# Kernel optimization log

Measured on AMD Instinct MI355X. Metric: run time of the kernel, lower is better.

Reference implementation:

```python
import jax, jax.numpy as jnp
import numpy as np

B, D, Nh, L = 8, 128, 8, 1024
Dk = D // Nh  # 16
Dv = D // Nh  # 16

def _xavier(key, shape):
    # nn.init.xavier_normal_ on a 3D tensor treats dim0 as fan irrelevant:
    # fan_in = shape[-1]*1, fan_out = shape[-2]*1 for >=2D; receptive field = prod(shape[2:])? For 3D torch uses
    # fan_in = shape[1]*shape[2]? We just need same distribution family; use std from last two dims.
    fan_in, fan_out = shape[-1], shape[-2]
    std = float(np.sqrt(2.0 / (fan_in + fan_out)))
    return jax.random.normal(key, shape, dtype=jnp.float32) * std

def setup_inputs() -> dict:
    key = jax.random.key(0)
    kx, kq, kk, kv, ko = jax.random.split(key, 5)
    x = jax.random.normal(kx, (B, D, L), dtype=jnp.float32)
    Wq = _xavier(kq, (Nh, B, Dk, D))
    Wk = _xavier(kk, (Nh, B, Dk, D))
    Wv = _xavier(kv, (Nh, B, Dv, D))
    Wo = _xavier(ko, (B, Dv * Nh, D))
    return {"x": x, "Wq": Wq, "Wk": Wk, "Wv": Wv, "Wo": Wo}

def reference(x, Wq, Wk, Wv, Wo):
    scale = 1.0 / np.sqrt(Dk)
    # Project all heads at once: [Nh,B,Dk,D] x [B,D,L] -> [B,Nh,Dk,L]
    Q = jnp.einsum('hbkd,bdl->bhkl', Wq, x)
    K = jnp.einsum('hbkd,bdl->bhkl', Wk, x)
    V = jnp.einsum('hbvd,bdl->bhvl', Wv, x)
    # scores[b,h,i,j] = sum_k Q[b,h,k,i] * K[b,h,k,j]
    scores = jnp.einsum('bhki,bhkj->bhij', Q, K) * scale
    # original softmaxes over dim=1 of [B,L,L] -> the i (Q-length) axis
    attn = jax.nn.softmax(scores, axis=2)
    # head[b,h,v,j] = sum_i V[b,h,v,i] * attn[b,h,i,j]
    head = jnp.einsum('bhvi,bhij->bhvj', V, attn)
    # concat heads along channel dim (order matches torch.cat over head list)
    head = head.reshape(B, Nh * Dv, L)
    # Wo [B, Nh*Dv, D] bmm head [B, D(=Nh*Dv), L] -> [B, Nh*Dv, L]
    out = jnp.einsum('bod,bdl->bol', Wo, head)
    return out
```

## Files before the change

kernel.cpp:

```cpp
#include <hip/hip_runtime.h>
#include <hip/hip_bf16.h>

#define B_ 8
#define D_ 128
#define NH 8
#define L_ 1024
#define DK 16

typedef __attribute__((ext_vector_type(4))) short s4;
typedef __attribute__((ext_vector_type(4))) float f4;

static __device__ __forceinline__ unsigned short f2bf(float f) {
    __hip_bfloat16 h = __float2bfloat16(f);
    return *reinterpret_cast<unsigned short*>(&h);
}
static __device__ __forceinline__ unsigned pack2(float a, float b) {
    return (unsigned)f2bf(a) | ((unsigned)f2bf(b) << 16);
}
static __device__ __forceinline__ s4 pack4(float a, float b, float c, float d) {
    union { unsigned u[2]; s4 v; } un;
    un.u[0] = pack2(a, b);
    un.u[1] = pack2(c, d);
    return un.v;
}

static __device__ __forceinline__ float fexp2(float x) {
#if __has_builtin(__builtin_amdgcn_exp2f)
    return __builtin_amdgcn_exp2f(x);
#else
    float r; asm("v_exp_f32 %0, %1" : "=v"(r) : "v"(x)); return r;
#endif
}

#if __has_builtin(__builtin_amdgcn_mfma_f32_16x16x16_bf16)
#define MFMA16(a, b, c) __builtin_amdgcn_mfma_f32_16x16x16_bf16(a, b, c, 0, 0, 0)
#elif __has_builtin(__builtin_amdgcn_mfma_f32_16x16x16bf16_1k)
#define MFMA16(a, b, c) __builtin_amdgcn_mfma_f32_16x16x16bf16_1k(a, b, c, 0, 0, 0)
#else
static __device__ __forceinline__ f4 mfma16_asm(s4 a, s4 b, f4 c) {
    f4 d;
    asm volatile("v_mfma_f32_16x16x16_bf16 %0, %1, %2, %3"
                 : "=&v"(d) : "v"(a), "v"(b), "v"(c));
    return d;
}
#define MFMA16(a, b, c) mfma16_asm(a, b, c)
#endif

__global__ __launch_bounds__(256)
void proj_kernel(const float* __restrict__ x,
                 const float* __restrict__ Wq,
                 const float* __restrict__ Wk,
                 const float* __restrict__ Wv,
                 unsigned short* __restrict__ Qt,
                 unsigned short* __restrict__ Kt,
                 unsigned short* __restrict__ Vt) {
    const int lane = threadIdx.x & 63;
    const int wv   = threadIdx.x >> 6;
    const int m = lane & 15, q = lane >> 4;
    const int bh = blockIdx.y, b = bh >> 3, h = bh & 7;
    const int which = blockIdx.z;
    const int n0 = (blockIdx.x * 4 + wv) * 32;

    const float* W = (which == 0) ? Wq : (which == 1) ? Wk : Wv;
    const float* Wrow = W + ((size_t)((h * B_ + b) * DK + m)) * D_;
    const float* xb = x + (size_t)b * D_ * L_ + n0 + m;

    f4 acc0 = {0.f, 0.f, 0.f, 0.f}, acc1 = {0.f, 0.f, 0.f, 0.f};
#pragma unroll
    for (int kb = 0; kb < 8; ++kb) {
        const int k4 = kb * 16 + q * 4;
        float4 wf = *(const float4*)(Wrow + k4);
        s4 a = pack4(wf.x, wf.y, wf.z, wf.w);

        const float* xc = xb + (size_t)k4 * L_;
        float b00 = xc[0];          float b01 = xc[L_];
        float b02 = xc[2 * L_];     float b03 = xc[3 * L_];
        float b10 = xc[16];         float b11 = xc[L_ + 16];
        float b12 = xc[2 * L_ + 16];float b13 = xc[3 * L_ + 16];
        s4 bf0 = pack4(b00, b01, b02, b03);
        s4 bf1 = pack4(b10, b11, b12, b13);

        acc0 = MFMA16(a, bf0, acc0);
        acc1 = MFMA16(a, bf1, acc1);
    }

    if (which == 2) {
        unsigned short* vp = Vt + ((size_t)bh * DK + q * 4) * L_ + n0 + m;
        vp[0]      = f2bf(acc0[0]); vp[L_]     = f2bf(acc0[1]);
        vp[2 * L_] = f2bf(acc0[2]); vp[3 * L_] = f2bf(acc0[3]);
        vp += 16;
        vp[0]      = f2bf(acc1[0]); vp[L_]     = f2bf(acc1[1]);
        vp[2 * L_] = f2bf(acc1[2]); vp[3 * L_] = f2bf(acc1[3]);
    } else {
        const float sc = (which == 1) ? 0.25f * 1.4426950408889634f : 1.0f;
        unsigned short* T = (which == 0) ? Qt : Kt;
        uint2 u0, u1;
        u0.x = pack2(acc0[0] * sc, acc0[1] * sc);
        u0.y = pack2(acc0[2] * sc, acc0[3] * sc);
        u1.x = pack2(acc1[0] * sc, acc1[1] * sc);
        u1.y = pack2(acc1[2] * sc, acc1[3] * sc);
        *(uint2*)(T + ((size_t)bh * L_ + n0 + m) * DK + q * 4)      = u0;
        *(uint2*)(T + ((size_t)bh * L_ + n0 + 16 + m) * DK + q * 4) = u1;
    }
}

__global__ __launch_bounds__(1024)
void attn_out_kernel(const unsigned short* __restrict__ Qt,
                     const unsigned short* __restrict__ Kt,
                     const unsigned short* __restrict__ Vt,
                     const float* __restrict__ Wo,
                     float* __restrict__ out) {
    const int lane = threadIdx.x & 63;
    const int wid  = threadIdx.x >> 6;
    const int m = lane & 15, q = lane >> 4;
    const int b    = blockIdx.y;
    const int jblk = blockIdx.x * 32;

    const int h     = wid & 7;
    const int ihalf = wid >> 3;
    const int bh    = b * NH + h;

    __shared__ unsigned short hls[32][132];
    __shared__ float red[8][64][12];

    s4 bk0 = *(const s4*)(Kt + ((size_t)bh * L_ + jblk + m) * DK + q * 4);
    s4 bk1 = *(const s4*)(Kt + ((size_t)bh * L_ + jblk + 16 + m) * DK + q * 4);

    f4 O0 = {0.f, 0.f, 0.f, 0.f}, O1 = {0.f, 0.f, 0.f, 0.f};
    float ls0 = 0.f, ls1 = 0.f;
    const unsigned short* qbase = Qt + (size_t)bh * L_ * DK + q * 4
                                     + (size_t)(ihalf * (L_ / 2)) * DK;
    const unsigned short* vbase = Vt + ((size_t)bh * DK + m) * L_ + q * 4
                                     + ihalf * (L_ / 2);

#pragma unroll 4
    for (int i0 = 0; i0 < L_ / 2; i0 += 16) {
        s4 aq = *(const s4*)(qbase + (size_t)(i0 + m) * DK);
        s4 av = *(const s4*)(vbase + i0);

        f4 z = {0.f, 0.f, 0.f, 0.f};
        f4 S0 = MFMA16(aq, bk0, z);
        f4 S1 = MFMA16(aq, bk1, z);

        float p00 = fexp2(S0[0]), p01 = fexp2(S0[1]);
        float p02 = fexp2(S0[2]), p03 = fexp2(S0[3]);
        float p10 = fexp2(S1[0]), p11 = fexp2(S1[1]);
        float p12 = fexp2(S1[2]), p13 = fexp2(S1[3]);
        ls0 += (p00 + p01) + (p02 + p03);
        ls1 += (p10 + p11) + (p12 + p13);

        s4 pb0, pb1;
        pb0[0] = (short)f2bf(p00); pb0[1] = (short)f2bf(p01);
        pb0[2] = (short)f2bf(p02); pb0[3] = (short)f2bf(p03);
        pb1[0] = (short)f2bf(p10); pb1[1] = (short)f2bf(p11);
        pb1[2] = (short)f2bf(p12); pb1[3] = (short)f2bf(p13);

        O0 = MFMA16(av, pb0, O0);
        O1 = MFMA16(av, pb1, O1);
    }

    ls0 += __shfl_xor(ls0, 16, 64);
    ls0 += __shfl_xor(ls0, 32, 64);
    ls1 += __shfl_xor(ls1, 16, 64);
    ls1 += __shfl_xor(ls1, 32, 64);

    if (ihalf) {
        float* r = red[h][lane];
        *(f4*)(r)     = O0;
        *(f4*)(r + 4) = O1;
        r[8] = ls0; r[9] = ls1;
    }
    __syncthreads();
    if (!ihalf) {
        const float* r = red[h][lane];
        f4 P0 = *(const f4*)(r), P1 = *(const f4*)(r + 4);
        O0 += P0; O1 += P1;
        const float inv0 = 1.f / (ls0 + r[8]);
        const float inv1 = 1.f / (ls1 + r[9]);

        uint2 o0, o1;
        o0.x = pack2(O0[0] * inv0, O0[1] * inv0);
        o0.y = pack2(O0[2] * inv0, O0[3] * inv0);
        o1.x = pack2(O1[0] * inv1, O1[1] * inv1);
        o1.y = pack2(O1[2] * inv1, O1[3] * inv1);
        *(uint2*)&hls[m][h * 16 + q * 4]      = o0;
        *(uint2*)&hls[16 + m][h * 16 + q * 4] = o1;
    }
    __syncthreads();

    {
        const int oc = wid & 7, jt = wid >> 3;
        const int o0 = oc * 16;
        const float* Wrow = Wo + ((size_t)b * D_ + o0 + m) * D_;

        f4 acc = {0.f, 0.f, 0.f, 0.f};
#pragma unroll
        for (int kb = 0; kb < 8; ++kb) {
            const int k4 = kb * 16 + q * 4;
            float4 wf = *(const float4*)(Wrow + k4);
            s4 a  = pack4(wf.x, wf.y, wf.z, wf.w);
            s4 bb = *(const s4*)&hls[jt * 16 + m][k4];
            acc = MFMA16(a, bb, acc);
        }

        float* op = out + ((size_t)b * D_ + o0 + q * 4) * L_ + jblk + jt * 16 + m;
        op[0]      = acc[0]; op[L_]     = acc[1];
        op[2 * L_] = acc[2]; op[3 * L_] = acc[3];
    }
}

extern "C" void kernel_launch(void* const* d_in, const int* in_sizes, int n_in,
                              void* d_out, int out_size, void* d_ws, size_t ws_size,
                              hipStream_t stream) {
    const float* x  = (const float*)d_in[0];
    const float* Wq = (const float*)d_in[1];
    const float* Wk = (const float*)d_in[2];
    const float* Wv = (const float*)d_in[3];
    const float* Wo = (const float*)d_in[4];
    float* out = (float*)d_out;

    const size_t SEG = (size_t)B_ * NH * DK * L_;
    unsigned short* Qt = (unsigned short*)d_ws;
    unsigned short* Kt = Qt + SEG;
    unsigned short* Vt = Kt + SEG;

    proj_kernel<<<dim3(8, B_ * NH, 3), 256, 0, stream>>>(x, Wq, Wk, Wv, Qt, Kt, Vt);
    attn_out_kernel<<<dim3(32, B_), 1024, 0, stream>>>(Qt, Kt, Vt, Wo, out);
}
```

Measured before the change: 99.58 us.

## Fuse QKV projections per block and halve attention j-tile for more blocks

The projection kernel now computes Q, K and V together in one block, reusing each loaded and packed x fragment across three MFMAs instead of launching a separate z-slice per projection. The attention kernel processes 16 output columns per block instead of 32, doubling the grid to 512 blocks so more of the GPU's compute units are busy. This trades lower per-block reuse (Q/V loads amortized over one key tile, Wo re-read twice as often, only half the waves doing the output GEMM) for more parallelism.

```diff
diff --git a/kernel.cpp b/kernel.cpp
--- a/kernel.cpp
+++ b/kernel.cpp
@@ -58,53 +58,52 @@
     const int wv   = threadIdx.x >> 6;
     const int m = lane & 15, q = lane >> 4;
     const int bh = blockIdx.y, b = bh >> 3, h = bh & 7;
-    const int which = blockIdx.z;
-    const int n0 = (blockIdx.x * 4 + wv) * 32;
-
-    const float* W = (which == 0) ? Wq : (which == 1) ? Wk : Wv;
-    const float* Wrow = W + ((size_t)((h * B_ + b) * DK + m)) * D_;
+    const int n0 = (blockIdx.x * 4 + wv) * 16;
+
+    const size_t wrow_off = ((size_t)((h * B_ + b) * DK + m)) * D_;
+    const float* Wqr = Wq + wrow_off;
+    const float* Wkr = Wk + wrow_off;
+    const float* Wvr = Wv + wrow_off;
     const float* xb = x + (size_t)b * D_ * L_ + n0 + m;
 
-    f4 acc0 = {0.f, 0.f, 0.f, 0.f}, acc1 = {0.f, 0.f, 0.f, 0.f};
+    f4 aQ = {0.f, 0.f, 0.f, 0.f}, aK = {0.f, 0.f, 0.f, 0.f}, aV = {0.f, 0.f, 0.f, 0.f};
 #pragma unroll
     for (int kb = 0; kb < 8; ++kb) {
         const int k4 = kb * 16 + q * 4;
-        float4 wf = *(const float4*)(Wrow + k4);
-        s4 a = pack4(wf.x, wf.y, wf.z, wf.w);
 
         const float* xc = xb + (size_t)k4 * L_;
-        float b00 = xc[0];          float b01 = xc[L_];
-        float b02 = xc[2 * L_];     float b03 = xc[3 * L_];
-        float b10 = xc[16];         float b11 = xc[L_ + 16];
-        float b12 = xc[2 * L_ + 16];float b13 = xc[3 * L_ + 16];
-        s4 bf0 = pack4(b00, b01, b02, b03);
-        s4 bf1 = pack4(b10, b11, b12, b13);
-
-        acc0 = MFMA16(a, bf0, acc0);
-        acc1 = MFMA16(a, bf1, acc1);
-    }
-
-    if (which == 2) {
-        unsigned short* vp = Vt + ((size_t)bh * DK + q * 4) * L_ + n0 + m;
-        vp[0]      = f2bf(acc0[0]); vp[L_]     = f2bf(acc0[1]);
-        vp[2 * L_] = f2bf(acc0[2]); vp[3 * L_] = f2bf(acc0[3]);
-        vp += 16;
-        vp[0]      = f2bf(acc1[0]); vp[L_]     = f2bf(acc1[1]);
-        vp[2 * L_] = f2bf(acc1[2]); vp[3 * L_] = f2bf(acc1[3]);
-    } else {
-        const float sc = (which == 1) ? 0.25f * 1.4426950408889634f : 1.0f;
-        unsigned short* T = (which == 0) ? Qt : Kt;
-        uint2 u0, u1;
-        u0.x = pack2(acc0[0] * sc, acc0[1] * sc);
-        u0.y = pack2(acc0[2] * sc, acc0[3] * sc);
-        u1.x = pack2(acc1[0] * sc, acc1[1] * sc);
-        u1.y = pack2(acc1[2] * sc, acc1[3] * sc);
-        *(uint2*)(T + ((size_t)bh * L_ + n0 + m) * DK + q * 4)      = u0;
-        *(uint2*)(T + ((size_t)bh * L_ + n0 + 16 + m) * DK + q * 4) = u1;
-    }
-}
-
-__global__ __launch_bounds__(1024)
+        float b0 = xc[0], b1 = xc[L_], b2 = xc[2 * L_], b3 = xc[3 * L_];
+        s4 bf = pack4(b0, b1, b2, b3);
+
+        float4 wq = *(const float4*)(Wqr + k4);
+        float4 wk = *(const float4*)(Wkr + k4);
+        float4 wv4 = *(const float4*)(Wvr + k4);
+        s4 fq = pack4(wq.x, wq.y, wq.z, wq.w);
+        s4 fk = pack4(wk.x, wk.y, wk.z, wk.w);
+        s4 fv = pack4(wv4.x, wv4.y, wv4.z, wv4.w);
+
+        aQ = MFMA16(fq, bf, aQ);
+        aK = MFMA16(fk, bf, aK);
+        aV = MFMA16(fv, bf, aV);
+    }
+
+    uint2 uq;
+    uq.x = pack2(aQ[0], aQ[1]);
+    uq.y = pack2(aQ[2], aQ[3]);
+    *(uint2*)(Qt + ((size_t)bh * L_ + n0 + m) * DK + q * 4) = uq;
+
+    const float sc = 0.25f * 1.4426950408889634f;
+    uint2 uk;
+    uk.x = pack2(aK[0] * sc, aK[1] * sc);
+    uk.y = pack2(aK[2] * sc, aK[3] * sc);
+    *(uint2*)(Kt + ((size_t)bh * L_ + n0 + m) * DK + q * 4) = uk;
+
+    unsigned short* vp = Vt + ((size_t)bh * DK + q * 4) * L_ + n0 + m;
+    vp[0]      = f2bf(aV[0]); vp[L_]     = f2bf(aV[1]);
+    vp[2 * L_] = f2bf(aV[2]); vp[3 * L_] = f2bf(aV[3]);
+}
+
+__global__ __launch_bounds__(1024, 8)
 void attn_out_kernel(const unsigned short* __restrict__ Qt,
                      const unsigned short* __restrict__ Kt,
                      const unsigned short* __restrict__ Vt,
@@ -114,83 +113,67 @@
     const int wid  = threadIdx.x >> 6;
     const int m = lane & 15, q = lane >> 4;
     const int b    = blockIdx.y;
-    const int jblk = blockIdx.x * 32;
+    const int jblk = blockIdx.x * 16;
 
     const int h     = wid & 7;
     const int ihalf = wid >> 3;
     const int bh    = b * NH + h;
 
-    __shared__ unsigned short hls[32][132];
-    __shared__ float red[8][64][12];
-
-    s4 bk0 = *(const s4*)(Kt + ((size_t)bh * L_ + jblk + m) * DK + q * 4);
-    s4 bk1 = *(const s4*)(Kt + ((size_t)bh * L_ + jblk + 16 + m) * DK + q * 4);
-
-    f4 O0 = {0.f, 0.f, 0.f, 0.f}, O1 = {0.f, 0.f, 0.f, 0.f};
-    float ls0 = 0.f, ls1 = 0.f;
+    __shared__ unsigned short hls[16][132];
+    __shared__ float red[8][64][8];
+
+    s4 bk = *(const s4*)(Kt + ((size_t)bh * L_ + jblk + m) * DK + q * 4);
+
+    f4 O = {0.f, 0.f, 0.f, 0.f};
+    float ls = 0.f;
     const unsigned short* qbase = Qt + (size_t)bh * L_ * DK + q * 4
                                      + (size_t)(ihalf * (L_ / 2)) * DK;
     const unsigned short* vbase = Vt + ((size_t)bh * DK + m) * L_ + q * 4
                                      + ihalf * (L_ / 2);
 
-#pragma unroll 4
+#pragma unroll 2
     for (int i0 = 0; i0 < L_ / 2; i0 += 16) {
         s4 aq = *(const s4*)(qbase + (size_t)(i0 + m) * DK);
         s4 av = *(const s4*)(vbase + i0);
 
         f4 z = {0.f, 0.f, 0.f, 0.f};
-        f4 S0 = MFMA16(aq, bk0, z);
-        f4 S1 = MFMA16(aq, bk1, z);
-
-        float p00 = fexp2(S0[0]), p01 = fexp2(S0[1]);
-        float p02 = fexp2(S0[2]), p03 = fexp2(S0[3]);
-        float p10 = fexp2(S1[0]), p11 = fexp2(S1[1]);
-        float p12 = fexp2(S1[2]), p13 = fexp2(S1[3]);
-        ls0 += (p00 + p01) + (p02 + p03);
-        ls1 += (p10 + p11) + (p12 + p13);
-
-        s4 pb0, pb1;
-        pb0[0] = (short)f2bf(p00); pb0[1] = (short)f2bf(p01);
-        pb0[2] = (short)f2bf(p02); pb0[3] = (short)f2bf(p03);
-        pb1[0] = (short)f2bf(p10); pb1[1] = (short)f2bf(p11);
-        pb1[2] = (short)f2bf(p12); pb1[3] = (short)f2bf(p13);
-
-        O0 = MFMA16(av, pb0, O0);
-        O1 = MFMA16(av, pb1, O1);
-    }
-
-    ls0 += __shfl_xor(ls0, 16, 64);
-    ls0 += __shfl_xor(ls0, 32, 64);
-    ls1 += __shfl_xor(ls1, 16, 64);
-    ls1 += __shfl_xor(ls1, 32, 64);
+        f4 S = MFMA16(aq, bk, z);
+
+        float p0 = fexp2(S[0]), p1 = fexp2(S[1]);
+        float p2 = fexp2(S[2]), p3 = fexp2(S[3]);
+        ls += (p0 + p1) + (p2 + p3);
+
+        s4 pb;
+        pb[0] = (short)f2bf(p0); pb[1] = (short)f2bf(p1);
+        pb[2] = (short)f2bf(p2); pb[3] = (short)f2bf(p3);
+
+        O = MFMA16(av, pb, O);
+    }
+
+    ls += __shfl_xor(ls, 16, 64);
+    ls += __shfl_xor(ls, 32, 64);
 
     if (ihalf) {
         float* r = red[h][lane];
-        *(f4*)(r)     = O0;
-        *(f4*)(r + 4) = O1;
-        r[8] = ls0; r[9] = ls1;
+        *(f4*)(r) = O;
+        r[4] = ls;
     }
     __syncthreads();
     if (!ihalf) {
         const float* r = red[h][lane];
-        f4 P0 = *(const f4*)(r), P1 = *(const f4*)(r + 4);
-        O0 += P0; O1 += P1;
-        const float inv0 = 1.f / (ls0 + r[8]);
-        const float inv1 = 1.f / (ls1 + r[9]);
-
-        uint2 o0, o1;
-        o0.x = pack2(O0[0] * inv0, O0[1] * inv0);
-        o0.y = pack2(O0[2] * inv0, O0[3] * inv0);
-        o1.x = pack2(O1[0] * inv1, O1[1] * inv1);
-        o1.y = pack2(O1[2] * inv1, O1[3] * inv1);
-        *(uint2*)&hls[m][h * 16 + q * 4]      = o0;
-        *(uint2*)&hls[16 + m][h * 16 + q * 4] = o1;
+        f4 P = *(const f4*)(r);
+        O += P;
+        const float inv = 1.f / (ls + r[4]);
+
+        uint2 o0;
+        o0.x = pack2(O[0] * inv, O[1] * inv);
+        o0.y = pack2(O[2] * inv, O[3] * inv);
+        *(uint2*)&hls[m][h * 16 + q * 4] = o0;
     }
     __syncthreads();
 
-    {
-        const int oc = wid & 7, jt = wid >> 3;
-        const int o0 = oc * 16;
+    if (wid < 8) {
+        const int o0 = wid * 16;
         const float* Wrow = Wo + ((size_t)b * D_ + o0 + m) * D_;
 
         f4 acc = {0.f, 0.f, 0.f, 0.f};
@@ -199,11 +182,11 @@
             const int k4 = kb * 16 + q * 4;
             float4 wf = *(const float4*)(Wrow + k4);
             s4 a  = pack4(wf.x, wf.y, wf.z, wf.w);
-            s4 bb = *(const s4*)&hls[jt * 16 + m][k4];
+            s4 bb = *(const s4*)&hls[m][k4];
             acc = MFMA16(a, bb, acc);
         }
 
-        float* op = out + ((size_t)b * D_ + o0 + q * 4) * L_ + jblk + jt * 16 + m;
+        float* op = out + ((size_t)b * D_ + o0 + q * 4) * L_ + jblk + m;
         op[0]      = acc[0]; op[L_]     = acc[1];
         op[2 * L_] = acc[2]; op[3 * L_] = acc[3];
     }
@@ -224,6 +207,6 @@
     unsigned short* Kt = Qt + SEG;
     unsigned short* Vt = Kt + SEG;
 
-    proj_kernel<<<dim3(8, B_ * NH, 3), 256, 0, stream>>>(x, Wq, Wk, Wv, Qt, Kt, Vt);
-    attn_out_kernel<<<dim3(32, B_), 1024, 0, stream>>>(Qt, Kt, Vt, Wo, out);
-}
+    proj_kernel<<<dim3(16, B_ * NH), 256, 0, stream>>>(x, Wq, Wk, Wv, Qt, Kt, Vt);
+    attn_out_kernel<<<dim3(64, B_), 1024, 0, stream>>>(Qt, Kt, Vt, Wo, out);
+}
```

Result: slower. 119.2 us (+19.7%).
